# Kernel optimization log

Measured on AMD Instinct MI355X. Metric: run time of the kernel, lower is better.

## Reference

```python
import jax, jax.numpy as jnp
import numpy as np

B, T, D, H, DK, DV = 2, 2048, 1024, 16, 64, 64
_MASK_ADDER = -10000.0  # tf-models MaskedSoftmax convention


def setup_inputs() -> dict:
    key = jax.random.key(0)
    ks = jax.random.split(key, 8)
    s = 0.02
    return {
        "query": jax.random.normal(ks[0], (B, T, D), jnp.float32),
        "value": jax.random.normal(ks[1], (B, T, D), jnp.float32),
        "Wq": jax.random.normal(ks[2], (D, H, DK), jnp.float32) * s,
        "bq": jnp.zeros((H, DK), jnp.float32),
        "Wk": jax.random.normal(ks[3], (D, H, DK), jnp.float32) * s,
        "bk": jnp.zeros((H, DK), jnp.float32),
        "Wv": jax.random.normal(ks[4], (D, H, DV), jnp.float32) * s,
        "bv": jnp.zeros((H, DV), jnp.float32),
        "Wo": jax.random.normal(ks[5], (H, DV, D), jnp.float32) * s,
        "bo": jnp.zeros((D,), jnp.float32),
        "attention_mask": jnp.ones((B, T, T), jnp.int32),
    }


def reference(query, value, Wq, bq, Wk, bk, Wv, bv, Wo, bo, attention_mask):
    # key defaults to value (call() with key=None); training=False -> no dropout
    q = jnp.einsum("btd,dhk->bthk", query, Wq) + bq          # [B,T,H,DK]
    k = jnp.einsum("bsd,dhk->bshk", value, Wk) + bk          # [B,S,H,DK]
    v = jnp.einsum("bsd,dhk->bshk", value, Wv) + bv          # [B,S,H,DV]
    q = q * (1.0 / jnp.sqrt(jnp.asarray(DK, q.dtype)))
    scores = jnp.einsum("bthk,bshk->bhts", q, k)             # [B,H,T,S]
    # MaskedSoftmax: expand mask at axis 1, additive -10000 on masked slots
    adder = (1.0 - attention_mask.astype(scores.dtype))[:, None, :, :] * _MASK_ADDER
    probs = jax.nn.softmax(scores + adder, axis=-1)
    ctx = jnp.einsum("bhts,bshv->bthv", probs, v)            # [B,T,H,DV]
    out = jnp.einsum("bthv,hvd->btd", ctx, Wo) + bo          # [B,T,D]
    return out
```

## Files before the change

### kernel.cpp

```cpp
#include <hip/hip_runtime.h>
#include <hip/hip_bf16.h>
#include <stdint.h>

#define TSEQ 2048
#define DMODEL 1024
#define NHEAD 16
#define HDIM 64
#define MROWS 4096
#define L2E 1.44269504088896340736f

typedef unsigned short u16;
typedef unsigned int u32;
typedef __attribute__((ext_vector_type(8))) short bf16x8;
typedef __attribute__((ext_vector_type(8))) unsigned short u16x8;
typedef __attribute__((ext_vector_type(4))) unsigned short u16x4;
typedef __attribute__((ext_vector_type(4))) float f32x4;
typedef __attribute__((ext_vector_type(16))) float f32x16;
typedef __attribute__((ext_vector_type(4))) unsigned int u32x4;

__device__ inline u16 f2bf(float f) {
  __hip_bfloat16 h(f);
  return __builtin_bit_cast(u16, h);
}

__device__ inline float fexp2(float x) { float r; asm("v_exp_f32 %0, %1" : "=v"(r) : "v"(x)); return r; }

__device__ inline unsigned cvtpk_bf16(float a, float b) {
  unsigned r; asm("v_cvt_pk_bf16_f32 %0, %1, %2" : "=v"(r) : "v"(a), "v"(b)); return r;
}

__device__ inline float fmax3(float a, float b, float c) {
  float r; asm("v_max3_f32 %0, %1, %2, %3" : "=v"(r) : "v"(a), "v"(b), "v"(c)); return r;
}

__device__ inline void permswap(u32& a, u32& b) {
  asm volatile("v_permlane32_swap_b32 %0, %1" : "+v"(a), "+v"(b));
}

__device__ inline void gload16(const void* g, void* l) {
  __builtin_amdgcn_global_load_lds((const __attribute__((address_space(1))) void*)g,
                                   (__attribute__((address_space(3))) void*)l, 16, 0, 0);
}

__global__ void prep(const float* __restrict__ q, const float* __restrict__ v,
                     u16* __restrict__ qo, u16* __restrict__ vo,
                     const float* __restrict__ Wq, const float* __restrict__ Wk,
                     const float* __restrict__ Wv, const float* __restrict__ Wo,
                     u16* __restrict__ WT3, u16* __restrict__ WoT,
                     const int* __restrict__ mask, int* __restrict__ flags) {
  __shared__ float tile[32][33];
  __shared__ int sred[4];
  const int bid = blockIdx.x, tid = threadIdx.x;
  if (bid < 8192) {
    const float* in = bid < 4096 ? q : v;
    u16* out = bid < 4096 ? qo : vo;
    const int i = (bid & 4095) * 1024 + tid * 4;
    float4 x = *(const float4*)(in + i);
    u16x4 o;
    o.x = f2bf(x.x); o.y = f2bf(x.y); o.z = f2bf(x.z); o.w = f2bf(x.w);
    *(u16x4*)(out + i) = o;
  } else if (bid < 12288) {
    int t = bid - 8192;
    const int z = t >> 10; t &= 1023;
    const float* W = z == 0 ? Wq : z == 1 ? Wk : z == 2 ? Wv : Wo;
    u16* WT = z < 3 ? (WT3 + (size_t)z * 1024 * 1024) : WoT;
    const int bx = t & 31, by = t >> 5;
    const int tr = tid >> 3;
    const int tc4 = (tid & 7) * 4;
    float4 x = *(const float4*)(W + (size_t)(by * 32 + tr) * 1024 + bx * 32 + tc4);
    tile[tr][tc4 + 0] = x.x; tile[tr][tc4 + 1] = x.y;
    tile[tr][tc4 + 2] = x.z; tile[tr][tc4 + 3] = x.w;
    __syncthreads();
    u16x4 o;
    o.x = f2bf(tile[tc4 + 0][tr]); o.y = f2bf(tile[tc4 + 1][tr]);
    o.z = f2bf(tile[tc4 + 2][tr]); o.w = f2bf(tile[tc4 + 3][tr]);
    *(u16x4*)(WT + (size_t)(bx * 32 + tr) * 1024 + by * 32 + tc4) = o;
  } else {
    const int t = bid - 12288;
    const int st = t & 15, qt = (t >> 4) & 15, b = t >> 8;
    const int row = qt * 128 + (tid >> 1);
    const int col0 = st * 128 + (tid & 1) * 64;
    const int* p = mask + (size_t)b * TSEQ * TSEQ + (size_t)row * TSEQ + col0;
    int ok = 1;
    #pragma unroll
    for (int j = 0; j < 64; j += 4) {
      int4 x = *(const int4*)(p + j);
      ok &= (x.x == 1) & (x.y == 1) & (x.z == 1) & (x.w == 1);
    }
    ok = __all(ok);
    if ((tid & 63) == 0) sred[tid >> 6] = ok;
    __syncthreads();
    if (tid == 0) flags[(b * 16 + qt) * 16 + st] = sred[0] & sred[1] & sred[2] & sred[3];
  }
}

__global__ __launch_bounds__(256) void gemm_qkv(
    const u16* __restrict__ qxb, const u16* __restrict__ vxb, const u16* __restrict__ WT3,
    const float* __restrict__ bq, const float* __restrict__ bk, const float* __restrict__ bv,
    u16* __restrict__ Qb, u16* __restrict__ Kb, u16* __restrict__ VTb, float qscale) {
  __shared__ u16 As[128 * 64];
  __shared__ u16 Bs[128 * 64];
  const int tid = threadIdx.x;
  const int w = tid >> 6, lane = tid & 63;
  const int lo = lane & 15, hi = lane >> 4;
  const int bid = blockIdx.x + (blockIdx.y << 5);
  const int swz = (bid & 7) * 96 + (bid >> 3);
  const int m0 = (swz & 31) << 7, n0 = (swz >> 5) << 7;
  const int nsel = n0 >> 10;
  const u16* A = nsel == 0 ? qxb : vxb;
  const float* bias = nsel == 0 ? bq : nsel == 1 ? bk : bv;
  const float scl = nsel == 0 ? qscale : 1.0f;
  const int wm = (w >> 1) * 64, wn = (w & 1) * 64;
  f32x4 acc[4][4] = {};
  const int loff = w * 4096 + lane * 16;
  for (int kt = 0; kt < 16; ++kt) {
    #pragma unroll
    for (int i = 0; i < 4; ++i) {
      const int off = loff + i * 1024;
      const int row = off >> 7;
      const int g = ((off >> 4) & 7) ^ (row & 7);
      gload16(A + (size_t)(m0 + row) * 1024 + kt * 64 + g * 8, (char*)As + off);
      gload16(WT3 + (size_t)(n0 + row) * 1024 + kt * 64 + g * 8, (char*)Bs + off);
    }
    __syncthreads();
    #pragma unroll
    for (int kk = 0; kk < 2; ++kk) {
      bf16x8 af[4], bfr[4];
      #pragma unroll
      for (int mi = 0; mi < 4; ++mi) {
        int row = wm + mi * 16 + lo;
        af[mi] = *(const bf16x8*)(As + row * 64 + (((kk * 4 + hi) ^ (row & 7)) << 3));
      }
      #pragma unroll
      for (int ni = 0; ni < 4; ++ni) {
        int row = wn + ni * 16 + lo;
        bfr[ni] = *(const bf16x8*)(Bs + row * 64 + (((kk * 4 + hi) ^ (row & 7)) << 3));
      }
      #pragma unroll
      for (int mi = 0; mi < 4; ++mi)
        #pragma unroll
        for (int ni = 0; ni < 4; ++ni)
          acc[mi][ni] = __builtin_amdgcn_mfma_f32_16x16x32_bf16(af[mi], bfr[ni], acc[mi][ni], 0, 0, 0);
    }
    __syncthreads();
  }
  if (nsel < 2) {
    u16* dst = nsel == 0 ? Qb : Kb;
    #pragma unroll
    for (int ni = 0; ni < 4; ++ni) {
      const int col = (n0 + wn + ni * 16 + lo) & 1023;
      const float bc = bias[col];
      #pragma unroll
      for (int mi = 0; mi < 4; ++mi) {
        #pragma unroll
        for (int r = 0; r < 4; ++r) {
          const int row = m0 + wm + mi * 16 + hi * 4 + r;
          const float v = (acc[mi][ni][r] + bc) * scl;
          dst[(size_t)(((row >> 11) * NHEAD + (col >> 6)) * TSEQ + (row & 2047)) * HDIM + (col & 63)] = f2bf(v);
        }
      }
    }
  } else {
    #pragma unroll
    for (int ni = 0; ni < 4; ++ni) {
      const int col = (n0 + wn + ni * 16 + lo) & 1023;
      const float bc = bias[col];
      const int v = col & 63;
      #pragma unroll
      for (int mi = 0; mi < 4; ++mi) {
        const int rowb = m0 + wm + mi * 16 + hi * 4;
        const int bh2 = (rowb >> 11) * NHEAD + (col >> 6);
        u16x4 pk;
        #pragma unroll
        for (int r = 0; r < 4; ++r) pk[r] = f2bf(acc[mi][ni][r] + bc);
        *(u16x4*)(VTb + ((size_t)bh2 * 64 + v) * TSEQ + (rowb & 2047)) = pk;
      }
    }
  }
}

__global__ __launch_bounds__(256) void gemm_o(const u16* __restrict__ A, const u16* __restrict__ BT,
                                              const float* __restrict__ bias, float* __restrict__ C) {
  __shared__ u16 As[64 * 64];
  __shared__ u16 Bs[128 * 64];
  const int tid = threadIdx.x;
  const int w = tid >> 6, lane = tid & 63;
  const int lo = lane & 15, hi = lane >> 4;
  const int bid = blockIdx.x + (blockIdx.y << 6);
  const int swz = (bid & 7) * 64 + (bid >> 3);
  const int m0 = (swz & 63) << 6, n0 = (swz >> 6) << 7;
  const int wm = (w >> 1) * 32, wn = (w & 1) * 64;
  f32x4 acc[2][4] = {};
  for (int kt = 0; kt < 16; ++kt) {
    #pragma unroll
    for (int i = 0; i < 2; ++i) {
      const int off = tid * 16 + i * 4096;
      const int row = off >> 7;
      const int g = ((off >> 4) & 7) ^ (row & 7);
      gload16(A + (size_t)(m0 + row) * 1024 + kt * 64 + g * 8, (char*)As + off);
    }
    #pragma unroll
    for (int i = 0; i < 4; ++i) {
      const int off = tid * 16 + i * 4096;
      const int row = off >> 7;
      const int g = ((off >> 4) & 7) ^ (row & 7);
      gload16(BT + (size_t)(n0 + row) * 1024 + kt * 64 + g * 8, (char*)Bs + off);
    }
    __syncthreads();
    #pragma unroll
    for (int kk = 0; kk < 2; ++kk) {
      bf16x8 af[2], bfr[4];
      #pragma unroll
      for (int mi = 0; mi < 2; ++mi) {
        int row = wm + mi * 16 + lo;
        af[mi] = *(const bf16x8*)(As + row * 64 + (((kk * 4 + hi) ^ (row & 7)) << 3));
      }
      #pragma unroll
      for (int ni = 0; ni < 4; ++ni) {
        int row = wn + ni * 16 + lo;
        bfr[ni] = *(const bf16x8*)(Bs + row * 64 + (((kk * 4 + hi) ^ (row & 7)) << 3));
      }
      #pragma unroll
      for (int mi = 0; mi < 2; ++mi)
        #pragma unroll
        for (int ni = 0; ni < 4; ++ni)
          acc[mi][ni] = __builtin_amdgcn_mfma_f32_16x16x32_bf16(af[mi], bfr[ni], acc[mi][ni], 0, 0, 0);
    }
    __syncthreads();
  }
  #pragma unroll
  for (int ni = 0; ni < 4; ++ni) {
    const int col = n0 + wn + ni * 16 + lo;
    const float bc = bias[col];
    #pragma unroll
    for (int mi = 0; mi < 2; ++mi)
      #pragma unroll
      for (int r = 0; r < 4; ++r) {
        const int row = m0 + wm + mi * 16 + hi * 4 + r;
        C[(size_t)row * DMODEL + col] = acc[mi][ni][r] + bc;
      }
  }
}

__global__ __launch_bounds__(256) void flash(
    const u16* __restrict__ Q, const u16* __restrict__ K, const u16* __restrict__ VT,
    const int* __restrict__ mask, const int* __restrict__ flags, u16* __restrict__ ctx) {
  __shared__ u16 Ks[2][64 * 64];
  __shared__ u16 Vs[3][64 * 64];
  const int tid = threadIdx.x, w = tid >> 6, lane = tid & 63;
  const int l5 = lane & 31, hi2 = lane >> 5;
  const int bid0 = blockIdx.x + (blockIdx.y << 4);
  const int swz = (bid0 & 7) * 64 + (bid0 >> 3);
  const int qt = swz & 15, bh = swz >> 4;
  const int b = bh >> 4, h = bh & 15;
  const int tq = qt * 128 + w * 32;

  const int soff = w * 2048 + lane * 16;
  const int srow0 = w * 16 + (lane >> 3);
  const int lg0 = (((lane & 7) ^ (lane >> 3) ^ ((w * 2) & 3)) << 3);
  const int lg1 = (((lane & 7) ^ (lane >> 3) ^ ((w * 2 + 1) & 3)) << 3);

  bf16x8 qf[4];
  #pragma unroll
  for (int kc = 0; kc < 4; ++kc)
    qf[kc] = *(const bf16x8*)(Q + ((size_t)bh * TSEQ + tq + l5) * 64 + kc * 16 + hi2 * 8);

  unsigned fl = 0;
  {
    const int* fp = flags + (b * 16 + qt) * 16;
    #pragma unroll
    for (int i = 0; i < 4; ++i) {
      int4 v = *(const int4*)(fp + i * 4);
      fl |= (unsigned)((v.x & 1) | ((v.y & 1) << 1) | ((v.z & 1) << 2) | ((v.w & 1) << 3)) << (4 * i);
    }
  }

  f32x16 o0 = {}, o1 = {};
  float mrow = -1e30f, lrow = 0.f;
  bf16x8 paA[4], paB[4];

#define STAGE_K(buf, st_) do {                                                        \
    const u16* kb_ = K + ((size_t)bh * TSEQ + (st_) * 64) * 64;                       \
    gload16(kb_ + (size_t)srow0 * 64 + lg0, (char*)Ks[buf] + soff);                   \
    gload16(kb_ + (size_t)(srow0 + 8) * 64 + lg1, (char*)Ks[buf] + soff + 1024);      \
  } while (0)
#define STAGE_V(buf, st_) do {                                                        \
    const u16* vb_ = VT + (size_t)bh * 64 * TSEQ + (st_) * 64;                        \
    gload16(vb_ + (size_t)srow0 * TSEQ + lg0, (char*)Vs[buf] + soff);                 \
    gload16(vb_ + (size_t)(srow0 + 8) * TSEQ + lg1, (char*)Vs[buf] + soff + 1024);    \
  } while (0)

#define FR(base, row, sg) \
  (*(const bf16x8*)((base) + (row) * 64 + ((((sg) ^ ((row) & 7) ^ (((row) >> 3) & 3)) << 3))))

#define QKC(T, S0, S1) do {                                                           \
    const u16* Kb_ = Ks[(T) & 1];                                                     \
    _Pragma("unroll") for (int kc = 0; kc < 4; ++kc) {                                \
      const int sg = kc * 2 + hi2;                                                    \
      S0 = __builtin_amdgcn_mfma_f32_32x32x16_bf16(FR(Kb_, l5, sg), qf[kc], S0, 0, 0, 0); \
      S1 = __builtin_amdgcn_mfma_f32_32x32x16_bf16(FR(Kb_, 32 + l5, sg), qf[kc], S1, 0, 0, 0); \
    } } while (0)

#define PVC(VB, PA) do {                                                              \
    const u16* Vb_ = Vs[VB];                                                          \
    _Pragma("unroll") for (int kc = 0; kc < 4; ++kc) {                                \
      const int sg = kc * 2 + hi2;                                                    \
      o0 = __builtin_amdgcn_mfma_f32_32x32x16_bf16(PA[kc], FR(Vb_, l5, sg), o0, 0, 0, 0); \
      o1 = __builtin_amdgcn_mfma_f32_32x32x16_bf16(PA[kc], FR(Vb_, 32 + l5, sg), o1, 0, 0, 0); \
    } } while (0)

#define SMAX(T, S0, S1, PAOUT) do {                                                   \
    if (!((fl >> ((T) >> 1)) & 1)) {                                                  \
      const int t_ = tq + l5;                                                         \
      const int* mp_ = mask + ((size_t)b * TSEQ + t_) * TSEQ + (T) * 64;              \
      _Pragma("unroll") for (int r = 0; r < 16; ++r) {                                \
        const int sr_ = (r & 3) + 8 * (r >> 2) + 4 * hi2;                             \
        S0[r] += (1.0f - (float)mp_[sr_]) * -14426.950408f;                           \
        S1[r] += (1.0f - (float)mp_[sr_ + 32]) * -14426.950408f;                      \
      } }                                                                             \
    float c0 = fmaxf(S0[0], S1[0]), c1 = fmaxf(S0[1], S1[1]);                         \
    float c2 = fmaxf(S0[2], S1[2]), c3 = fmaxf(S0[3], S1[3]);                         \
    _Pragma("unroll") for (int r = 4; r < 16; r += 4) {                               \
      c0 = fmax3(c0, S0[r], S1[r]);     c1 = fmax3(c1, S0[r+1], S1[r+1]);             \
      c2 = fmax3(c2, S0[r+2], S1[r+2]); c3 = fmax3(c3, S0[r+3], S1[r+3]); }           \
    float pm = fmax3(fmaxf(c0, c1), c2, c3);                                          \
    pm = fmaxf(pm, __shfl_xor(pm, 32));                                               \
    if (__any(pm - mrow > 11.0f)) {                                                   \
      const float mn_ = fmaxf(mrow, pm);                                              \
      const float a_ = fexp2(mrow - mn_);                                             \
      lrow *= a_; mrow = mn_;                                                         \
      _Pragma("unroll") for (int r = 0; r < 16; ++r) {                                \
        const float ar_ = __shfl(a_, (r & 3) + 8 * (r >> 2) + 4 * hi2);               \
        o0[r] *= ar_; o1[r] *= ar_; } }                                               \
    float rs = 0.f; u32 W0_[8], W1_[8];                                               \
    _Pragma("unroll") for (int q_ = 0; q_ < 4; ++q_)                                  \
      _Pragma("unroll") for (int c_ = 0; c_ < 2; ++c_) {                              \
        const int r = 4 * q_ + 2 * c_;                                                \
        float a0 = fexp2(S0[r] - mrow), b0 = fexp2(S0[r + 1] - mrow);                 \
        float a1 = fexp2(S1[r] - mrow), b1 = fexp2(S1[r + 1] - mrow);                 \
        rs += (a0 + b0) + (a1 + b1);                                                  \
        W0_[q_ * 2 + c_] = cvtpk_bf16(a0, b0);                                        \
        W1_[q_ * 2 + c_] = cvtpk_bf16(a1, b1); }                                      \
    rs += __shfl_xor(rs, 32); lrow += rs;                                             \
    _Pragma("unroll") for (int ts = 0; ts < 2; ++ts)                                  \
      _Pragma("unroll") for (int qp = 0; qp < 2; ++qp) {                              \
        u32 d0 = ts ? W1_[(2 * qp) * 2 + 0] : W0_[(2 * qp) * 2 + 0];                  \
        u32 e0 = ts ? W1_[(2 * qp + 1) * 2 + 0] : W0_[(2 * qp + 1) * 2 + 0];          \
        u32 d1 = ts ? W1_[(2 * qp) * 2 + 1] : W0_[(2 * qp) * 2 + 1];                  \
        u32 e1 = ts ? W1_[(2 * qp + 1) * 2 + 1] : W0_[(2 * qp + 1) * 2 + 1];          \
        permswap(d0, e0); permswap(d1, e1);                                           \
        u32x4 fw_; fw_.x = d0; fw_.y = d1; fw_.z = e0; fw_.w = e1;                    \
        PAOUT[ts * 2 + qp] = __builtin_bit_cast(bf16x8, fw_); }                       \
  } while (0)

#define BODY(T, VPREV, VNEXT, DOSTAGE, PAIN, PAOUT) do {                              \
    if (DOSTAGE) { STAGE_K(((T) + 1) & 1, (T) + 1); STAGE_V(VNEXT, (T) + 1); }        \
    f32x16 s0 = {}, s1 = {};                                                          \
    __builtin_amdgcn_s_setprio(1);                                                    \
    QKC(T, s0, s1);                                                                   \
    PVC(VPREV, PAIN);                                                                 \
    __builtin_amdgcn_s_setprio(0);                                                    \
    SMAX(T, s0, s1, PAOUT);                                                           \
    __syncthreads();                                                                  \
  } while (0)

  STAGE_K(0, 0); STAGE_V(0, 0);
  __syncthreads();
  {
    f32x16 s0 = {}, s1 = {};
    __builtin_amdgcn_s_setprio(1);
    QKC(0, s0, s1);
    __builtin_amdgcn_s_setprio(0);
    STAGE_K(1, 1); STAGE_V(1, 1);
    SMAX(0, s0, s1, paA);
    __syncthreads();
  }

  int vp = 0, vn = 2;
  for (int t = 1; t < 31; t += 2) {
    BODY(t, vp, vn, 1, paA, paB);
    const int vp2 = (vp + 1 == 3) ? 0 : vp + 1;
    const int vn2 = (vn + 1 == 3) ? 0 : vn + 1;
    BODY(t + 1, vp2, vn2, 1, paB, paA);
    vp = (vp2 + 1 == 3) ? 0 : vp2 + 1;
    vn = (vn2 + 1 == 3) ? 0 : vn2 + 1;
  }
  BODY(31, vp, 0, 0, paA, paB);

  __builtin_amdgcn_s_setprio(1);
  PVC(1, paB);
  __builtin_amdgcn_s_setprio(0);

#undef BODY
#undef SMAX
#undef PVC
#undef QKC
#undef FR
#undef STAGE_V
#undef STAGE_K

  const float inv = 1.0f / lrow;
  #pragma unroll
  for (int r = 0; r < 16; ++r) {
    const int sr = (r & 3) + 8 * (r >> 2) + 4 * hi2;
    const float ir = __shfl(inv, sr);
    u16* cp = ctx + (size_t)(b * TSEQ + tq + sr) * DMODEL + h * 64;
    cp[l5] = f2bf(o0[r] * ir);
    cp[32 + l5] = f2bf(o1[r] * ir);
  }
}

extern "C" void kernel_launch(void* const* d_in, const int* in_sizes, int n_in,
                              void* d_out, int out_size, void* d_ws, size_t ws_size,
                              hipStream_t stream) {
  (void)in_sizes; (void)n_in; (void)out_size; (void)ws_size;
  const float* query = (const float*)d_in[0];
  const float* value = (const float*)d_in[1];
  const float* Wq = (const float*)d_in[2];
  const float* bq = (const float*)d_in[3];
  const float* Wk = (const float*)d_in[4];
  const float* bk = (const float*)d_in[5];
  const float* Wv = (const float*)d_in[6];
  const float* bv = (const float*)d_in[7];
  const float* Wo = (const float*)d_in[8];
  const float* bo = (const float*)d_in[9];
  const int* amask = (const int*)d_in[10];

  char* ws = (char*)d_ws;
  const size_t MB = 1 << 20;
  u16* qxb = (u16*)(ws + 0 * MB);
  u16* vxb = (u16*)(ws + 8 * MB);
  u16* WT3 = (u16*)(ws + 16 * MB);
  u16* WoT = (u16*)(ws + 22 * MB);
  u16* Qb  = (u16*)(ws + 24 * MB);
  u16* Kb  = (u16*)(ws + 32 * MB);
  u16* VTb = (u16*)(ws + 48 * MB);
  u16* ctx = (u16*)(ws + 56 * MB);
  int* flg = (int*)(ws + 64 * MB);

  prep<<<12800, 256, 0, stream>>>(query, value, qxb, vxb, Wq, Wk, Wv, Wo, WT3, WoT, amask, flg);
  gemm_qkv<<<dim3(32, 24), 256, 0, stream>>>(qxb, vxb, WT3, bq, bk, bv, Qb, Kb, VTb, 0.125f * L2E);
  flash<<<dim3(16, 32), 256, 0, stream>>>(Qb, Kb, VTb, amask, flg, ctx);
  gemm_o<<<dim3(64, 8), 256, 0, stream>>>(ctx, WoT, bo, (float*)d_out);
}
```

Measured before the change: 144.0 us.

## Stage V-transpose through LDS and compute softmax row sums via MFMA

The V projection epilogue now writes the transposed tile into shared memory with an XOR swizzle, then emits 16-byte coalesced stores to the transposed V buffer instead of scattered 8-byte stores. In the flash kernel the per-row softmax denominator is accumulated by an extra MFMA against a ones vector, replacing scalar adds and a cross-lane shuffle. Workspace offsets are also rearranged so the flags and WoT buffers sit below 48 MB. The extra MFMA adds matrix work per tile and one more 16-float accumulator, which raises register pressure in the flash kernel.

```diff
diff --git a/kernel.cpp b/kernel.cpp
--- a/kernel.cpp
+++ b/kernel.cpp
@@ -98,8 +98,9 @@
     const u16* __restrict__ qxb, const u16* __restrict__ vxb, const u16* __restrict__ WT3,
     const float* __restrict__ bq, const float* __restrict__ bk, const float* __restrict__ bv,
     u16* __restrict__ Qb, u16* __restrict__ Kb, u16* __restrict__ VTb, float qscale) {
-  __shared__ u16 As[128 * 64];
-  __shared__ u16 Bs[128 * 64];
+  __shared__ u16 SMEM[2 * 128 * 64];
+  u16* As = SMEM;
+  u16* Bs = SMEM + 128 * 64;
   const int tid = threadIdx.x;
   const int w = tid >> 6, lane = tid & 63;
   const int lo = lane & 15, hi = lane >> 4;
@@ -161,20 +162,31 @@
       }
     }
   } else {
+    u16* T = SMEM;
     #pragma unroll
     for (int ni = 0; ni < 4; ++ni) {
-      const int col = (n0 + wn + ni * 16 + lo) & 1023;
-      const float bc = bias[col];
-      const int v = col & 63;
+      const int nl = wn + ni * 16 + lo;
+      const float bc = bias[(n0 + nl) & 1023];
       #pragma unroll
       for (int mi = 0; mi < 4; ++mi) {
-        const int rowb = m0 + wm + mi * 16 + hi * 4;
-        const int bh2 = (rowb >> 11) * NHEAD + (col >> 6);
+        const int mloc = wm + mi * 16 + hi * 4;
         u16x4 pk;
         #pragma unroll
         for (int r = 0; r < 4; ++r) pk[r] = f2bf(acc[mi][ni][r] + bc);
-        *(u16x4*)(VTb + ((size_t)bh2 * 64 + v) * TSEQ + (rowb & 2047)) = pk;
-      }
+        const int cg = mloc >> 3, sub = mloc & 7;
+        *(u16x4*)(T + nl * 128 + (((cg ^ (nl & 15)) << 3) + sub)) = pk;
+      }
+    }
+    __syncthreads();
+    const int b_ = m0 >> 11, t0_ = m0 & 2047;
+    #pragma unroll
+    for (int p = 0; p < 8; ++p) {
+      const int nl = p * 16 + (tid >> 4);
+      const int cg = tid & 15;
+      u16x8 val = *(const u16x8*)(T + nl * 128 + ((cg ^ (nl & 15)) << 3));
+      const int colg = (n0 + nl) & 1023;
+      u16* dst = VTb + ((size_t)(b_ * NHEAD + (colg >> 6)) * 64 + (colg & 63)) * TSEQ + t0_ + cg * 8;
+      *(u16x8*)dst = val;
     }
   }
 }
@@ -265,6 +277,10 @@
   for (int kc = 0; kc < 4; ++kc)
     qf[kc] = *(const bf16x8*)(Q + ((size_t)bh * TSEQ + tq + l5) * 64 + kc * 16 + hi2 * 8);
 
+  bf16x8 onesf;
+  #pragma unroll
+  for (int j = 0; j < 8; ++j) onesf[j] = (short)0x3F80;
+
   unsigned fl = 0;
   {
     const int* fp = flags + (b * 16 + qt) * 16;
@@ -275,8 +291,8 @@
     }
   }
 
-  f32x16 o0 = {}, o1 = {};
-  float mrow = -1e30f, lrow = 0.f;
+  f32x16 o0 = {}, o1 = {}, o2 = {};
+  float mrow = -1e30f;
   bf16x8 paA[4], paB[4];
 
 #define STAGE_K(buf, st_) do {                                                        \
@@ -307,6 +323,7 @@
       const int sg = kc * 2 + hi2;                                                    \
       o0 = __builtin_amdgcn_mfma_f32_32x32x16_bf16(PA[kc], FR(Vb_, l5, sg), o0, 0, 0, 0); \
       o1 = __builtin_amdgcn_mfma_f32_32x32x16_bf16(PA[kc], FR(Vb_, 32 + l5, sg), o1, 0, 0, 0); \
+      o2 = __builtin_amdgcn_mfma_f32_32x32x16_bf16(PA[kc], onesf, o2, 0, 0, 0);       \
     } } while (0)
 
 #define SMAX(T, S0, S1, PAOUT) do {                                                   \
@@ -328,20 +345,18 @@
     if (__any(pm - mrow > 11.0f)) {                                                   \
       const float mn_ = fmaxf(mrow, pm);                                              \
       const float a_ = fexp2(mrow - mn_);                                             \
-      lrow *= a_; mrow = mn_;                                                         \
+      mrow = mn_;                                                                     \
       _Pragma("unroll") for (int r = 0; r < 16; ++r) {                                \
         const float ar_ = __shfl(a_, (r & 3) + 8 * (r >> 2) + 4 * hi2);               \
-        o0[r] *= ar_; o1[r] *= ar_; } }                                               \
-    float rs = 0.f; u32 W0_[8], W1_[8];                                               \
+        o0[r] *= ar_; o1[r] *= ar_; o2[r] *= ar_; } }                                 \
+    u32 W0_[8], W1_[8];                                                               \
     _Pragma("unroll") for (int q_ = 0; q_ < 4; ++q_)                                  \
       _Pragma("unroll") for (int c_ = 0; c_ < 2; ++c_) {                              \
         const int r = 4 * q_ + 2 * c_;                                                \
         float a0 = fexp2(S0[r] - mrow), b0 = fexp2(S0[r + 1] - mrow);                 \
         float a1 = fexp2(S1[r] - mrow), b1 = fexp2(S1[r + 1] - mrow);                 \
-        rs += (a0 + b0) + (a1 + b1);                                                  \
         W0_[q_ * 2 + c_] = cvtpk_bf16(a0, b0);                                        \
         W1_[q_ * 2 + c_] = cvtpk_bf16(a1, b1); }                                      \
-    rs += __shfl_xor(rs, 32); lrow += rs;                                             \
     _Pragma("unroll") for (int ts = 0; ts < 2; ++ts)                                  \
       _Pragma("unroll") for (int qp = 0; qp < 2; ++qp) {                              \
         u32 d0 = ts ? W1_[(2 * qp) * 2 + 0] : W0_[(2 * qp) * 2 + 0];                  \
@@ -399,11 +414,10 @@
 #undef STAGE_V
 #undef STAGE_K
 
-  const float inv = 1.0f / lrow;
   #pragma unroll
   for (int r = 0; r < 16; ++r) {
     const int sr = (r & 3) + 8 * (r >> 2) + 4 * hi2;
-    const float ir = __shfl(inv, sr);
+    const float ir = 1.0f / o2[r];
     u16* cp = ctx + (size_t)(b * TSEQ + tq + sr) * DMODEL + h * 64;
     cp[l5] = f2bf(o0[r] * ir);
     cp[32 + l5] = f2bf(o1[r] * ir);
@@ -431,12 +445,12 @@
   u16* qxb = (u16*)(ws + 0 * MB);
   u16* vxb = (u16*)(ws + 8 * MB);
   u16* WT3 = (u16*)(ws + 16 * MB);
-  u16* WoT = (u16*)(ws + 22 * MB);
   u16* Qb  = (u16*)(ws + 24 * MB);
   u16* Kb  = (u16*)(ws + 32 * MB);
+  int* flg = (int*)(ws + 42 * MB);
+  u16* WoT = (u16*)(ws + 44 * MB);
   u16* VTb = (u16*)(ws + 48 * MB);
   u16* ctx = (u16*)(ws + 56 * MB);
-  int* flg = (int*)(ws + 64 * MB);
 
   prep<<<12800, 256, 0, stream>>>(query, value, qxb, vxb, Wq, Wk, Wv, Wo, WT3, WoT, amask, flg);
   gemm_qkv<<<dim3(32, 24), 256, 0, stream>>>(qxb, vxb, WT3, bq, bk, bv, Qb, Kb, VTb, 0.125f * L2E);
```

After: 142.9 us. Within noise of the previous version (-0.8%).
